# Optimization experiments

Hardware: AMD Instinct MI355X
Metric: run time of the kernel (lower is better)

## Reference

```python
import jax, jax.numpy as jnp
import numpy as np

S, D, H, HD, FF = 4096, 1024, 16, 64, 4096  # seq, d_embed, heads, head_dim, hidden
EPS = 1e-6  # flax LayerNorm default epsilon


def layer_norm(x, scale, bias):
    mu = jnp.mean(x, axis=-1, keepdims=True)
    var = jnp.var(x, axis=-1, keepdims=True)
    return (x - mu) * jax.lax.rsqrt(var + EPS) * scale + bias


def rope(x):
    # x: [S, H, HD]; standard half-split rotary embedding, base 10000
    half = x.shape[-1] // 2
    freq = 1.0 / (10000.0 ** (jnp.arange(half, dtype=x.dtype) / half))  # [half]
    ang = jnp.arange(x.shape[0], dtype=x.dtype)[:, None] * freq          # [S, half]
    cos = jnp.cos(ang)[:, None, :]
    sin = jnp.sin(ang)[:, None, :]
    x1, x2 = x[..., :half], x[..., half:]
    return jnp.concatenate([x1 * cos - x2 * sin, x2 * cos + x1 * sin], axis=-1)


def setup_inputs() -> dict:
    key = jax.random.key(0)
    ks = jax.random.split(key, 8)
    s = 0.02
    return {
        "x": jax.random.normal(ks[0], (S, D), jnp.float32),
        "ln1_scale": jnp.ones((D,), jnp.float32), "ln1_bias": jnp.zeros((D,), jnp.float32),
        "ln2_scale": jnp.ones((D,), jnp.float32), "ln2_bias": jnp.zeros((D,), jnp.float32),
        "Wq": jax.random.normal(ks[1], (D, H, HD), jnp.float32) * s, "bq": jnp.zeros((H, HD), jnp.float32),
        "Wk": jax.random.normal(ks[2], (D, H, HD), jnp.float32) * s, "bk": jnp.zeros((H, HD), jnp.float32),
        "Wv": jax.random.normal(ks[3], (D, H, HD), jnp.float32) * s, "bv": jnp.zeros((H, HD), jnp.float32),
        "Wo": jax.random.normal(ks[4], (H, HD, D), jnp.float32) * s, "bo": jnp.zeros((D,), jnp.float32),
        "W1": jax.random.normal(ks[5], (D, FF), jnp.float32) * s, "b1": jnp.zeros((FF,), jnp.float32),
        "W2": jax.random.normal(ks[6], (FF, D), jnp.float32) * s, "b2": jnp.zeros((D,), jnp.float32),
    }


def reference(x, ln1_scale, ln1_bias, ln2_scale, ln2_bias, Wq, bq, Wk, bk, Wv, bv, Wo, bo, W1, b1, W2, b2):
    # Pre-LN attention block with RoPE fused into QK scores
    y = layer_norm(x, ln1_scale, ln1_bias)
    q = jnp.einsum('sd,dhc->shc', y, Wq) + bq  # [S,H,HD]
    k = jnp.einsum('sd,dhc->shc', y, Wk) + bk
    v = jnp.einsum('sd,dhc->shc', y, Wv) + bv
    q = rope(q)
    k = rope(k)
    scores = jnp.einsum('qhc,khc->hqk', q, k) / jnp.sqrt(jnp.asarray(HD, x.dtype))  # [H,S,S]
    p = jax.nn.softmax(scores, axis=-1)
    o = jnp.einsum('hqk,khc->qhc', p, v)                # [S,H,HD]
    attn_out = jnp.einsum('qhc,hcd->qd', o, Wo) + bo    # [S,D]
    x = x + attn_out
    # Pre-LN GELU MLP block
    y = layer_norm(x, ln2_scale, ln2_bias)
    y = jax.nn.gelu(y @ W1 + b1, approximate=False)
    x = x + (y @ W2 + b2)
    return x
```

## Files before the change

### kernel.cpp

```cpp
#include <hip/hip_runtime.h>
#include <hip/hip_bf16.h>
#include <math.h>

using bf16 = __hip_bfloat16;
typedef __attribute__((ext_vector_type(8))) short short8;
typedef __attribute__((ext_vector_type(4))) short s16x4;
typedef __attribute__((ext_vector_type(4))) float f32x4;

constexpr int S = 4096, D = 1024, H = 16, HD = 64, FF = 4096;

static __device__ __forceinline__ float tof(bf16 v) { return __bfloat162float(v); }
static __device__ __forceinline__ bf16 tob(float v) { return __float2bfloat16(v); }
static __device__ __forceinline__ short tobs(float v) {
    bf16 h = __float2bfloat16(v);
    return *reinterpret_cast<short*>(&h);
}
static __device__ __forceinline__ unsigned pkbf16(float a, float b) {
    __hip_bfloat162 h = __float22bfloat162_rn(make_float2(a, b));
    return *reinterpret_cast<unsigned*>(&h);
}

#if __has_builtin(__builtin_amdgcn_exp2f)
#define EXP2(x) __builtin_amdgcn_exp2f(x)
#else
#define EXP2(x) exp2f(x)
#endif

static __device__ __forceinline__ f32x4 mfma16(short8 a, short8 b, f32x4 c) {
    return __builtin_amdgcn_mfma_f32_16x16x32_bf16(a, b, c, 0, 0, 0);
}
static __device__ __forceinline__ void stage16(const bf16* g, bf16* l) {
    __builtin_amdgcn_global_load_lds((__attribute__((address_space(1))) void*)g,
                                     (__attribute__((address_space(3))) void*)l, 16, 0, 0);
}
static __device__ __forceinline__ void pl32swap(unsigned& a, unsigned& b) {
    asm("v_permlane32_swap_b32 %0, %1" : "+v"(a), "+v"(b));
}
static __device__ __forceinline__ void pl16swap(unsigned& a, unsigned& b) {
    asm("v_permlane16_swap_b32 %0, %1" : "+v"(a), "+v"(b));
}

__global__ __launch_bounds__(256) void rope_tab(float2* __restrict__ tab) {
    int i = blockIdx.x * 256 + threadIdx.x;
    int s = i >> 5, dim = i & 31;
    float freq = __expf(-(float)dim * (9.210340371976184f / 32.f));
    float sn, cs;
    sincosf((float)s * freq, &sn, &cs);
    tab[i] = make_float2(cs, sn);
}

__global__ __launch_bounds__(256) void ln_kernel(const float* __restrict__ x,
                                                 const float* __restrict__ scale,
                                                 const float* __restrict__ bias,
                                                 bf16* __restrict__ y) {
    int row = blockIdx.x, t = threadIdx.x;
    const float* xr = x + (size_t)row * D;
    float v[4], s = 0.f, ss = 0.f;
#pragma unroll
    for (int i = 0; i < 4; ++i) {
        v[i] = xr[t + 256 * i];
        s += v[i]; ss += v[i] * v[i];
    }
    __shared__ float r0[256], r1[256];
    r0[t] = s; r1[t] = ss;
    __syncthreads();
    for (int off = 128; off; off >>= 1) {
        if (t < off) { r0[t] += r0[t + off]; r1[t] += r1[t + off]; }
        __syncthreads();
    }
    float mu  = r0[0] * (1.f / D);
    float var = r1[0] * (1.f / D) - mu * mu;
    float inv = rsqrtf(var + 1e-6f);
    bf16* yr = y + (size_t)row * D;
#pragma unroll
    for (int i = 0; i < 4; ++i) {
        int c = t + 256 * i;
        yr[c] = tob((v[i] - mu) * inv * scale[c] + bias[c]);
    }
}

__global__ __launch_bounds__(256) void wtrans_all(
    const float* __restrict__ Wq, const float* __restrict__ Wk,
    const float* __restrict__ Wv, const float* __restrict__ Wo,
    const float* __restrict__ W1, const float* __restrict__ W2,
    const float* __restrict__ bq, const float* __restrict__ bk,
    const float* __restrict__ bv,
    bf16* __restrict__ BTqkv, bf16* __restrict__ BTo,
    bf16* __restrict__ BT1, bf16* __restrict__ BT2, float* __restrict__ bqkv) {
    int id = blockIdx.x;
    if (id >= 12288) {
        int i = (id - 12288) * 256 + threadIdx.x;
        bqkv[i] = i < 1024 ? bq[i] : (i < 2048 ? bk[i - 1024] : bv[i - 2048]);
        return;
    }
    const float* W; bf16* dst; int K, N, local;
    if (id < 3072)      { int s = id >> 10; W = s == 0 ? Wq : (s == 1 ? Wk : Wv);
                          dst = BTqkv + (size_t)s * 1048576; K = 1024; N = 1024; local = id & 1023; }
    else if (id < 4096) { W = Wo; dst = BTo; K = 1024; N = 1024; local = id - 3072; }
    else if (id < 8192) { W = W1; dst = BT1; K = 1024; N = 4096; local = id - 4096; }
    else                { W = W2; dst = BT2; K = 4096; N = 1024; local = id - 8192; }
    int ls = (N == 4096) ? 7 : 5;
    int nt = (local & ((1 << ls) - 1)) << 5, kt = (local >> ls) << 5;
    __shared__ float t[32][33];
    int tid = threadIdx.x, r = tid >> 5, c = tid & 31;
#pragma unroll
    for (int p = 0; p < 4; ++p)
        t[r + p * 8][c] = W[(size_t)(kt + r + p * 8) * N + nt + c];
    __syncthreads();
#pragma unroll
    for (int p = 0; p < 4; ++p)
        dst[(size_t)(nt + r + p * 8) * K + kt + c] = tob(t[c][r + p * 8]);
}

#define EPI_RES  1
#define EPI_GELU 2
#define EPI_QKV  3

template <int EPI, int MT>
__global__ __launch_bounds__(256, MT == 128 ? 2 : 3) void gemm_bt(
    const bf16* __restrict__ A, const bf16* __restrict__ BT,
    const float* __restrict__ bias, const float* resid, void* out, void* out2,
    int M, int N, int K, int kLen) {
    constexpr int NJ = (MT == 128) ? 4 : 2;
    __shared__ bf16 As[2][MT * 32];
    __shared__ bf16 Bs[2][128 * 32];
    const int tid = threadIdx.x;
    const int w = tid >> 6, lane = tid & 63;
    const int quad = lane >> 4, l16 = lane & 15;
    const int rowBase = blockIdx.y * MT, colBase = blockIdx.x * 128;
    const int kStart = blockIdx.z * kLen;
    const int wr = (MT == 128) ? (w >> 1) * 64 : 0;
    const int wc = (MT == 128) ? (w & 1) * 64 : w * 32;
    const int sr = lane >> 2;
    const int skb = (((lane & 3) ^ ((lane >> 3) & 3)) * 8);
    const int fr = (l16 >> 1) & 3;
    f32x4 acc[4][NJ] = {};

    auto stage = [&](int k0, int b) {
        if constexpr (MT == 128) {
#pragma unroll
            for (int t = 0; t < 2; ++t) {
                int inst = w * 2 + t;
                int r = inst * 16 + sr;
                stage16(A  + (size_t)(rowBase + r) * K + kStart + k0 + skb, &As[b][inst * 512]);
                stage16(BT + (size_t)(colBase + r) * K + kStart + k0 + skb, &Bs[b][inst * 512]);
            }
        } else {
            stage16(A + (size_t)(rowBase + w * 16 + sr) * K + kStart + k0 + skb, &As[b][w * 512]);
#pragma unroll
            for (int t = 0; t < 2; ++t) {
                int inst = w + t * 4;
                stage16(BT + (size_t)(colBase + inst * 16 + sr) * K + kStart + k0 + skb, &Bs[b][inst * 512]);
            }
        }
    };

    stage(0, 0);
    const int nSteps = kLen >> 5;
    for (int s = 0; s < nSteps; ++s) {
        const int cb = s & 1;
        __builtin_amdgcn_s_barrier();
        if (s + 1 < nSteps) {
            stage((s + 1) << 5, cb ^ 1);
            if constexpr (MT == 128) asm volatile("s_waitcnt vmcnt(4)" ::: "memory");
            else                     asm volatile("s_waitcnt vmcnt(3)" ::: "memory");
        } else {
            asm volatile("s_waitcnt vmcnt(0)" ::: "memory");
        }
        __builtin_amdgcn_s_barrier();
        const bf16* pa = &As[cb][(wr + l16) * 32 + (quad ^ fr) * 8];
        const bf16* pb = &Bs[cb][(wc + l16) * 32 + (quad ^ fr) * 8];
        short8 a[4], b[NJ];
#pragma unroll
        for (int i = 0; i < 4; ++i) a[i] = *(const short8*)(pa + i * 512);
#pragma unroll
        for (int j = 0; j < NJ; ++j) b[j] = *(const short8*)(pb + j * 512);
#pragma unroll
        for (int i = 0; i < 4; ++i)
#pragma unroll
            for (int j = 0; j < NJ; ++j) acc[i][j] = mfma16(a[i], b[j], acc[i][j]);
    }
    if (EPI == EPI_QKV) {
        bf16* QKo = (bf16*)out;
        bf16* VTo = (bf16*)out2;
        if (colBase >= 2048) {
            bf16* tb = (bf16*)&As[0][0];
            const int cp = (w & 1) * 16 + l16;
            const int rr = tid >> 3, cb8 = (tid & 7) * 16;
#pragma unroll
            for (int j = 0; j < NJ; ++j) {
                int cg = colBase + (w & 1) * 64 + j * 16 + l16;
                float bj = bias[cg];
                __syncthreads();
#pragma unroll
                for (int i = 0; i < 4; ++i) {
                    int sp = (w >> 1) * 64 + i * 16 + quad * 4;
                    s16x4 pv = {tobs(acc[i][j][0] + bj), tobs(acc[i][j][1] + bj),
                                tobs(acc[i][j][2] + bj), tobs(acc[i][j][3] + bj)};
                    *(s16x4*)(tb + cp * 136 + sp) = pv;
                }
                __syncthreads();
                short8 v0 = *(const short8*)(tb + rr * 136 + cb8);
                short8 v1 = *(const short8*)(tb + rr * 136 + cb8 + 8);
                int cg2 = colBase - 2048 + (rr >> 4) * 64 + j * 16 + (rr & 15);
                bf16* dst = VTo + (size_t)cg2 * 4096 + rowBase + cb8;
                *(short8*)dst = v0;
                *(short8*)(dst + 8) = v1;
            }
        } else {
            const bool isq = colBase < 1024;
            const float qs = isq ? 0.125f * 1.44269504088896f : 1.f;
            const float2* tab = (const float2*)resid;
#pragma unroll
            for (int j2 = 0; j2 < 2; ++j2) {
                int dim = j2 * 16 + l16;
                int c1 = colBase + wc + j2 * 16 + l16, c2 = c1 + 32;
                float b1v = bias[c1], b2v = bias[c2];
#pragma unroll
                for (int i = 0; i < 4; ++i) {
#pragma unroll
                    for (int reg = 0; reg < 4; ++reg) {
                        int s = rowBase + wr + i * 16 + quad * 4 + reg;
                        float2 t = tab[s * 32 + dim];
                        float x1 = acc[i][j2][reg] + b1v;
                        float x2 = acc[i][j2 + 2][reg] + b2v;
                        QKo[(size_t)s * 2048 + c1] = tob((x1 * t.x - x2 * t.y) * qs);
                        QKo[(size_t)s * 2048 + c2] = tob((x2 * t.x + x1 * t.y) * qs);
                    }
                }
            }
        }
    } else {
#pragma unroll
        for (int j = 0; j < NJ; ++j) {
            int c = colBase + wc + j * 16 + l16;
            float bj = bias[c];
#pragma unroll
            for (int i = 0; i < 4; ++i) {
                int r0 = rowBase + wr + i * 16 + quad * 4;
#pragma unroll
                for (int reg = 0; reg < 4; ++reg) {
                    size_t idx = (size_t)(r0 + reg) * N + c;
                    float val = acc[i][j][reg] + bj;
                    if (EPI == EPI_RES) {
                        ((float*)out)[idx] = val + resid[idx];
                    } else {
                        float g = 0.5f * val * (1.f + erff(val * 0.70710678118f));
                        ((bf16*)out)[idx] = tob(g);
                    }
                }
            }
        }
    }
}

__global__ __launch_bounds__(256, 2) void attn_kernel(const bf16* __restrict__ QK,
                                                      const bf16* __restrict__ VT,
                                                      bf16* __restrict__ o) {
    const int bx = blockIdx.x;
    const int h = bx >> 5, qb = bx & 31;
    const int w = threadIdx.x >> 6, lane = threadIdx.x & 63;
    const int quad = lane >> 4, l16 = lane & 15;
    const int q0w = qb * 128 + w * 32;
    const bf16* Qh = QK + h * 64;
    const bf16* Kh = QK + 1024 + h * 64;
    const bf16* Vh = VT + (size_t)h * 64 * 4096;

    __shared__ char smem[32768];

    const int sw = l16 & 7;
    const int rloc = lane >> 3, slot = lane & 7;
    const int schunk = (slot ^ rloc) * 8;
    const int row0 = w * 16 + rloc, row1 = w * 16 + 8 + rloc;

    short8 qf[2][2];
#pragma unroll
    for (int qt = 0; qt < 2; ++qt)
#pragma unroll
        for (int c = 0; c < 2; ++c)
            qf[qt][c] = *(const short8*)(Qh + (size_t)(q0w + qt * 16 + l16) * 2048 + c * 32 + quad * 8);

    const short ob = (l16 == 0) ? (short)0x3F80 : (short)0;
    const short8 ones8 = {ob, ob, ob, ob, ob, ob, ob, ob};

    f32x4 acc[4][2] = {};
    f32x4 accl[2] = {};
    const f32x4 zero = {0.f, 0.f, 0.f, 0.f};

    {
        bf16* Ksb = (bf16*)smem;
        bf16* Vsb = (bf16*)(smem + 8192);
        stage16(Kh + (size_t)row0 * 2048 + schunk, Ksb + w * 1024);
        stage16(Kh + (size_t)row1 * 2048 + schunk, Ksb + w * 1024 + 512);
        stage16(Vh + (size_t)row0 * 4096 + schunk, Vsb + w * 1024);
        stage16(Vh + (size_t)row1 * 4096 + schunk, Vsb + w * 1024 + 512);
    }

#pragma unroll 2
    for (int t = 0; t < 64; ++t) {
        char* curb = smem + (t & 1) * 16384;
        char* nxtb = smem + ((t + 1) & 1) * 16384;
        __builtin_amdgcn_s_barrier();
        if (t < 63) {
            const int ktA = (t + 1) * 64;
            bf16* Ksb = (bf16*)nxtb;
            bf16* Vsb = (bf16*)(nxtb + 8192);
            stage16(Kh + (size_t)(ktA + row0) * 2048 + schunk, Ksb + w * 1024);
            stage16(Kh + (size_t)(ktA + row1) * 2048 + schunk, Ksb + w * 1024 + 512);
            stage16(Vh + (size_t)row0 * 4096 + ktA + schunk, Vsb + w * 1024);
            stage16(Vh + (size_t)row1 * 4096 + ktA + schunk, Vsb + w * 1024 + 512);
            asm volatile("s_waitcnt vmcnt(4)" ::: "memory");
        } else {
            asm volatile("s_waitcnt vmcnt(0)" ::: "memory");
        }
        __builtin_amdgcn_s_barrier();

        const bf16* Ks = (const bf16*)curb;
        const bf16* Vs = (const bf16*)(curb + 8192);

        unsigned u[4][2][2];
#pragma unroll
        for (int nt = 0; nt < 4; ++nt) {
            const bf16* kr = Ks + (nt * 16 + l16) * 64;
            short8 k0 = *(const short8*)(kr + ((quad ^ sw) * 8));
            short8 k1 = *(const short8*)(kr + (((quad + 4) ^ sw) * 8));
#pragma unroll
            for (int qt = 0; qt < 2; ++qt) {
                f32x4 st = mfma16(k1, qf[qt][1], mfma16(k0, qf[qt][0], zero));
                u[nt][qt][0] = pkbf16(EXP2(st[0]), EXP2(st[1]));
                u[nt][qt][1] = pkbf16(EXP2(st[2]), EXP2(st[3]));
            }
        }
#pragma unroll
        for (int c = 0; c < 2; ++c) {
            short8 pB[2];
#pragma unroll
            for (int qt = 0; qt < 2; ++qt) {
                unsigned a0 = u[2 * c][qt][0], a1 = u[2 * c][qt][1];
                unsigned b0 = u[2 * c + 1][qt][0], b1 = u[2 * c + 1][qt][1];
                pl32swap(a0, b0);
                pl32swap(a1, b1);
                pl16swap(a0, b0);
                pl16swap(a1, b1);
                union { unsigned u4[4]; short8 s8; } pk;
                pk.u4[0] = a0; pk.u4[1] = a1; pk.u4[2] = b0; pk.u4[3] = b1;
                pB[qt] = pk.s8;
                accl[qt] = mfma16(ones8, pB[qt], accl[qt]);
            }
#pragma unroll
            for (int vt = 0; vt < 4; ++vt) {
                short8 vf = *(const short8*)(Vs + (vt * 16 + l16) * 64 + (((c * 4 + quad) ^ sw) * 8));
#pragma unroll
                for (int qt = 0; qt < 2; ++qt)
                    acc[vt][qt] = mfma16(vf, pB[qt], acc[vt][qt]);
            }
        }
    }
#pragma unroll
    for (int qt = 0; qt < 2; ++qt) {
        float lq = __shfl(accl[qt][0], l16, 64);
        float linv = 1.f / lq;
        int q = q0w + qt * 16 + l16;
#pragma unroll
        for (int vt = 0; vt < 4; ++vt) {
            s16x4 ov = {tobs(acc[vt][qt][0] * linv), tobs(acc[vt][qt][1] * linv),
                        tobs(acc[vt][qt][2] * linv), tobs(acc[vt][qt][3] * linv)};
            *(s16x4*)(o + (size_t)q * 1024 + h * 64 + vt * 16 + quad * 4) = ov;
        }
    }
}

extern "C" void kernel_launch(void* const* d_in, const int* in_sizes, int n_in,
                              void* d_out, int out_size, void* d_ws, size_t ws_size,
                              hipStream_t stream) {
    const float* x   = (const float*)d_in[0];
    const float* s1  = (const float*)d_in[1];
    const float* b1n = (const float*)d_in[2];
    const float* s2  = (const float*)d_in[3];
    const float* b2n = (const float*)d_in[4];
    const float* Wq  = (const float*)d_in[5];
    const float* bq  = (const float*)d_in[6];
    const float* Wk  = (const float*)d_in[7];
    const float* bk  = (const float*)d_in[8];
    const float* Wv  = (const float*)d_in[9];
    const float* bv  = (const float*)d_in[10];
    const float* Wo  = (const float*)d_in[11];
    const float* bo  = (const float*)d_in[12];
    const float* W1  = (const float*)d_in[13];
    const float* b1  = (const float*)d_in[14];
    const float* W2  = (const float*)d_in[15];
    const float* b2  = (const float*)d_in[16];

    char* ws = (char*)d_ws;
    bf16*  y    = (bf16*)(ws);
    bf16*  QK   = (bf16*)(ws + (8ull  << 20));
    bf16*  BTo  = (bf16*)(ws + (24ull << 20));
    float* bqkv = (float*)(ws + (27ull << 20));
    float2* tab = (float2*)(ws + (28ull << 20));
    bf16*  o    = (bf16*)(ws + (32ull << 20));
    bf16*  hb   = (bf16*)(ws + (40ull << 20));
    bf16*  BTqkv= (bf16*)(ws + (40ull << 20));
    bf16*  VT   = (bf16*)(ws + (72ull << 20));
    bf16*  BT1  = (bf16*)(ws + (80ull << 20));
    bf16*  BT2  = (bf16*)(ws + (88ull << 20));
    float* x1   = (float*)d_out;

    wtrans_all<<<12300, 256, 0, stream>>>(Wq, Wk, Wv, Wo, W1, W2, bq, bk, bv,
                                          BTqkv, BTo, BT1, BT2, bqkv);

    rope_tab<<<512, 256, 0, stream>>>(tab);

    ln_kernel<<<S, 256, 0, stream>>>(x, s1, b1n, y);

    gemm_bt<EPI_QKV, 128><<<dim3(24, 32), 256, 0, stream>>>(y, BTqkv, bqkv, (const float*)tab, QK, VT, S, 3072, D, D);

    attn_kernel<<<H * 32, 256, 0, stream>>>(QK, VT, o);

    gemm_bt<EPI_RES, 64><<<dim3(8, 64), 256, 0, stream>>>(o, BTo, bo, x, x1, nullptr, S, D, D, D);

    ln_kernel<<<S, 256, 0, stream>>>(x1, s2, b2n, y);

    gemm_bt<EPI_GELU, 128><<<dim3(32, 32), 256, 0, stream>>>(y, BT1, b1, nullptr, hb, nullptr, S, FF, D, D);

    gemm_bt<EPI_RES, 64><<<dim3(8, 64), 256, 0, stream>>>(hb, BT2, b2, x1, x1, nullptr, S, D, FF, FF);
}
```

Baseline: 416.3 us.

## Widen GEMM K-tile to 64, remap blocks across XCDs, compute RoPE inline

```diff
diff --git a/kernel.cpp b/kernel.cpp
--- a/kernel.cpp
+++ b/kernel.cpp
@@ -38,15 +38,6 @@
 }
 static __device__ __forceinline__ void pl16swap(unsigned& a, unsigned& b) {
     asm("v_permlane16_swap_b32 %0, %1" : "+v"(a), "+v"(b));
-}
-
-__global__ __launch_bounds__(256) void rope_tab(float2* __restrict__ tab) {
-    int i = blockIdx.x * 256 + threadIdx.x;
-    int s = i >> 5, dim = i & 31;
-    float freq = __expf(-(float)dim * (9.210340371976184f / 32.f));
-    float sn, cs;
-    sincosf((float)s * freq, &sn, &cs);
-    tab[i] = make_float2(cs, sn);
 }
 
 __global__ __launch_bounds__(256) void ln_kernel(const float* __restrict__ x,
@@ -122,63 +113,66 @@
     const float* __restrict__ bias, const float* resid, void* out, void* out2,
     int M, int N, int K, int kLen) {
     constexpr int NJ = (MT == 128) ? 4 : 2;
-    __shared__ bf16 As[2][MT * 32];
-    __shared__ bf16 Bs[2][128 * 32];
+    __shared__ bf16 As[2][MT * 64];
+    __shared__ bf16 Bs[2][128 * 64];
     const int tid = threadIdx.x;
     const int w = tid >> 6, lane = tid & 63;
     const int quad = lane >> 4, l16 = lane & 15;
-    const int rowBase = blockIdx.y * MT, colBase = blockIdx.x * 128;
+    const int gx = gridDim.x, nwg = gx * gridDim.y;
+    int bid = blockIdx.y * gx + blockIdx.x;
+    bid = (bid & 7) * (nwg >> 3) + (bid >> 3);
+    const int rowBase = (bid / gx) * MT, colBase = (bid % gx) * 128;
     const int kStart = blockIdx.z * kLen;
     const int wr = (MT == 128) ? (w >> 1) * 64 : 0;
     const int wc = (MT == 128) ? (w & 1) * 64 : w * 32;
-    const int sr = lane >> 2;
-    const int skb = (((lane & 3) ^ ((lane >> 3) & 3)) * 8);
-    const int fr = (l16 >> 1) & 3;
+    const int swk = l16 & 7;
     f32x4 acc[4][NJ] = {};
 
     auto stage = [&](int k0, int b) {
-        if constexpr (MT == 128) {
-#pragma unroll
-            for (int t = 0; t < 2; ++t) {
-                int inst = w * 2 + t;
-                int r = inst * 16 + sr;
-                stage16(A  + (size_t)(rowBase + r) * K + kStart + k0 + skb, &As[b][inst * 512]);
-                stage16(BT + (size_t)(colBase + r) * K + kStart + k0 + skb, &Bs[b][inst * 512]);
-            }
-        } else {
-            stage16(A + (size_t)(rowBase + w * 16 + sr) * K + kStart + k0 + skb, &As[b][w * 512]);
-#pragma unroll
-            for (int t = 0; t < 2; ++t) {
-                int inst = w + t * 4;
-                stage16(BT + (size_t)(colBase + inst * 16 + sr) * K + kStart + k0 + skb, &Bs[b][inst * 512]);
-            }
+#pragma unroll
+        for (int i = 0; i < MT / 32; ++i) {
+            int s = i * 256 + tid;
+            int row = s >> 3, gch = ((s & 7) ^ (row & 7)) * 8;
+            stage16(A + (size_t)(rowBase + row) * K + kStart + k0 + gch,
+                    &As[b][i * 2048 + w * 512]);
+        }
+#pragma unroll
+        for (int i = 0; i < 4; ++i) {
+            int s = i * 256 + tid;
+            int row = s >> 3, gch = ((s & 7) ^ (row & 7)) * 8;
+            stage16(BT + (size_t)(colBase + row) * K + kStart + k0 + gch,
+                    &Bs[b][i * 2048 + w * 512]);
         }
     };
 
     stage(0, 0);
-    const int nSteps = kLen >> 5;
+    const int nSteps = kLen >> 6;
     for (int s = 0; s < nSteps; ++s) {
         const int cb = s & 1;
         __builtin_amdgcn_s_barrier();
         if (s + 1 < nSteps) {
-            stage((s + 1) << 5, cb ^ 1);
-            if constexpr (MT == 128) asm volatile("s_waitcnt vmcnt(4)" ::: "memory");
-            else                     asm volatile("s_waitcnt vmcnt(3)" ::: "memory");
+            stage((s + 1) << 6, cb ^ 1);
+            if constexpr (MT == 128) asm volatile("s_waitcnt vmcnt(8)" ::: "memory");
+            else                     asm volatile("s_waitcnt vmcnt(6)" ::: "memory");
         } else {
             asm volatile("s_waitcnt vmcnt(0)" ::: "memory");
         }
         __builtin_amdgcn_s_barrier();
-        const bf16* pa = &As[cb][(wr + l16) * 32 + (quad ^ fr) * 8];
-        const bf16* pb = &Bs[cb][(wc + l16) * 32 + (quad ^ fr) * 8];
-        short8 a[4], b[NJ];
-#pragma unroll
-        for (int i = 0; i < 4; ++i) a[i] = *(const short8*)(pa + i * 512);
-#pragma unroll
-        for (int j = 0; j < NJ; ++j) b[j] = *(const short8*)(pb + j * 512);
-#pragma unroll
-        for (int i = 0; i < 4; ++i)
-#pragma unroll
-            for (int j = 0; j < NJ; ++j) acc[i][j] = mfma16(a[i], b[j], acc[i][j]);
+        const bf16* pa = &As[cb][(wr + l16) * 64];
+        const bf16* pb = &Bs[cb][(wc + l16) * 64];
+#pragma unroll
+        for (int half = 0; half < 2; ++half) {
+            const int co = ((half * 4 + quad) ^ swk) * 8;
+            short8 a[4], b[NJ];
+#pragma unroll
+            for (int i = 0; i < 4; ++i) a[i] = *(const short8*)(pa + i * 1024 + co);
+#pragma unroll
+            for (int j = 0; j < NJ; ++j) b[j] = *(const short8*)(pb + j * 1024 + co);
+#pragma unroll
+            for (int i = 0; i < 4; ++i)
+#pragma unroll
+                for (int j = 0; j < NJ; ++j) acc[i][j] = mfma16(a[i], b[j], acc[i][j]);
+        }
     }
     if (EPI == EPI_QKV) {
         bf16* QKo = (bf16*)out;
@@ -210,10 +204,10 @@
         } else {
             const bool isq = colBase < 1024;
             const float qs = isq ? 0.125f * 1.44269504088896f : 1.f;
-            const float2* tab = (const float2*)resid;
 #pragma unroll
             for (int j2 = 0; j2 < 2; ++j2) {
                 int dim = j2 * 16 + l16;
+                float freq = __expf(-(float)dim * (9.210340371976184f / 32.f));
                 int c1 = colBase + wc + j2 * 16 + l16, c2 = c1 + 32;
                 float b1v = bias[c1], b2v = bias[c2];
 #pragma unroll
@@ -221,11 +215,12 @@
 #pragma unroll
                     for (int reg = 0; reg < 4; ++reg) {
                         int s = rowBase + wr + i * 16 + quad * 4 + reg;
-                        float2 t = tab[s * 32 + dim];
+                        float sn, cs;
+                        sincosf((float)s * freq, &sn, &cs);
                         float x1 = acc[i][j2][reg] + b1v;
                         float x2 = acc[i][j2 + 2][reg] + b2v;
-                        QKo[(size_t)s * 2048 + c1] = tob((x1 * t.x - x2 * t.y) * qs);
-                        QKo[(size_t)s * 2048 + c2] = tob((x2 * t.x + x1 * t.y) * qs);
+                        QKo[(size_t)s * 2048 + c1] = tob((x1 * cs - x2 * sn) * qs);
+                        QKo[(size_t)s * 2048 + c2] = tob((x2 * cs + x1 * sn) * qs);
                     }
                 }
             }
@@ -396,7 +391,6 @@
     bf16*  QK   = (bf16*)(ws + (8ull  << 20));
     bf16*  BTo  = (bf16*)(ws + (24ull << 20));
     float* bqkv = (float*)(ws + (27ull << 20));
-    float2* tab = (float2*)(ws + (28ull << 20));
     bf16*  o    = (bf16*)(ws + (32ull << 20));
     bf16*  hb   = (bf16*)(ws + (40ull << 20));
     bf16*  BTqkv= (bf16*)(ws + (40ull << 20));
@@ -408,11 +402,9 @@
     wtrans_all<<<12300, 256, 0, stream>>>(Wq, Wk, Wv, Wo, W1, W2, bq, bk, bv,
                                           BTqkv, BTo, BT1, BT2, bqkv);
 
-    rope_tab<<<512, 256, 0, stream>>>(tab);
-
     ln_kernel<<<S, 256, 0, stream>>>(x, s1, b1n, y);
 
-    gemm_bt<EPI_QKV, 128><<<dim3(24, 32), 256, 0, stream>>>(y, BTqkv, bqkv, (const float*)tab, QK, VT, S, 3072, D, D);
+    gemm_bt<EPI_QKV, 128><<<dim3(24, 32), 256, 0, stream>>>(y, BTqkv, bqkv, nullptr, QK, VT, S, 3072, D, D);
 
     attn_kernel<<<H * 32, 256, 0, stream>>>(QK, VT, o);
 
```

Result: no change. 410.2 us (-1.5%).
